# Performance work log

Hardware: AMD Instinct MI355X
Metric: run time of the kernel (lower is better)

## Reference

```python
import jax, jax.numpy as jnp
import numpy as np

B = 256          # batch_size (number of graphs)
N = 512          # padded nodes per graph
IN_FEATS = 74
DIM = 128
E = 1_048_576    # total edges in batched graph
N_NODES = B * N


def setup_inputs() -> dict:
    key = jax.random.key(0)
    ks = jax.random.split(key, 10)
    x = jax.random.normal(ks[0], (N_NODES, IN_FEATS), dtype=jnp.float32)
    src = jax.random.randint(ks[1], (E,), 0, N_NODES, dtype=jnp.int32)
    dst = jax.random.randint(ks[2], (E,), 0, N_NODES, dtype=jnp.int32)
    # init_transform: Linear(in_feats, dim_embedding, bias=False); padding=True
    # zeroes weight[-1] (last OUTPUT row) -> last column in [in, out] layout.
    W_init = jax.random.normal(ks[3], (IN_FEATS, DIM), dtype=jnp.float32) * 0.1
    W_init = W_init.at[:, -1].set(0.0)
    W1 = jax.random.normal(ks[4], (DIM, DIM), dtype=jnp.float32) * 0.1
    W2 = jax.random.normal(ks[5], (DIM, DIM), dtype=jnp.float32) * 0.1
    W3 = jax.random.normal(ks[6], (DIM, DIM), dtype=jnp.float32) * 0.1
    b1 = jnp.zeros((DIM,), dtype=jnp.float32)
    b2 = jnp.zeros((DIM,), dtype=jnp.float32)
    b3 = jnp.zeros((DIM,), dtype=jnp.float32)
    return {"x": x, "src": src, "dst": dst, "W_init": W_init,
            "W1": W1, "b1": b1, "W2": W2, "b2": b2, "W3": W3, "b3": b3}


def _gcn_forward(x, src, dst, W_init, Ws, bs):
    n = x.shape[0]
    h = x @ W_init                                    # [n, DIM] initial embedding
    ones = jnp.ones(src.shape[0], dtype=x.dtype)
    deg_out = jax.ops.segment_sum(ones, src, num_segments=n)
    deg_in = jax.ops.segment_sum(ones, dst, num_segments=n)
    nrm_src = jax.lax.rsqrt(jnp.clip(deg_out, 1.0))   # D_out^{-1/2}
    nrm_dst = jax.lax.rsqrt(jnp.clip(deg_in, 1.0))    # D_in^{-1/2}
    for W, b in zip(Ws, bs):
        m = (h * nrm_src[:, None])[src]               # gather normalized messages [E, DIM]
        agg = jax.ops.segment_sum(m, dst, num_segments=n)  # scatter-add to dst nodes
        h = jax.nn.relu((agg * nrm_dst[:, None]) @ W + b)
    return h.reshape(B, N, -1)                        # [B, N, output_feats]


def reference(x, src, dst, W_init, W1, b1, W2, b2, W3, b3):
    return _gcn_forward(x, src, dst, W_init, (W1, W2, W3), (b1, b2, b3))
```

## Files before the change

### kernel.cpp

```cpp
#include <hip/hip_runtime.h>

#define NN 131072
#define NE 1048576
#define OFF_DEG_OUT 0x000000
#define OFF_CURSOR  0x080000
#define OFF_WT      0x100000
#define OFF_WTI     0x118000
#define OFF_BUCKET  0x200000
#define OFF_HN      0x2200000

typedef __attribute__((ext_vector_type(8))) short bf16x8;
typedef __attribute__((ext_vector_type(4))) float f32x4;

static __device__ __forceinline__ float blo(unsigned u){ return __uint_as_float(u << 16); }
static __device__ __forceinline__ float bhi(unsigned u){ return __uint_as_float(u & 0xffff0000u); }
static __device__ __forceinline__ unsigned f2b(float f){
    unsigned u = __float_as_uint(f);
    return (u + 0x7fffu + ((u >> 16) & 1u)) >> 16;
}
static __device__ __forceinline__ unsigned pack2(float a, float b){
    return f2b(a) | (f2b(b) << 16);
}

__global__ __launch_bounds__(256) void k_fill(const int* __restrict__ src,
                                              const int* __restrict__ dst,
                                              int* __restrict__ deg_out,
                                              int* __restrict__ cursor,
                                              int* __restrict__ bucket) {
    int base = (blockIdx.x * 256 + threadIdx.x) * 2;
    int2 s2 = *(const int2*)&src[base];
    int2 d2 = *(const int2*)&dst[base];
    int p0 = atomicAdd(&cursor[d2.x], 1);
    int p1 = atomicAdd(&cursor[d2.y], 1);
    atomicAdd(&deg_out[s2.x], 1);
    atomicAdd(&deg_out[s2.y], 1);
    if (p0 < 64) bucket[(size_t)d2.x * 64 + p0] = s2.x;
    if (p1 < 64) bucket[(size_t)d2.y * 64 + p1] = s2.y;
}

__global__ __launch_bounds__(256) void k_wprep(const float* __restrict__ W1,
                                               const float* __restrict__ W2,
                                               const float* __restrict__ W3,
                                               const float* __restrict__ Wi,
                                               unsigned short* __restrict__ Wt,
                                               unsigned short* __restrict__ Wti) {
    int idx = blockIdx.x * 256 + threadIdx.x;
    if (idx < 49152) {
        int L = idx >> 14, rem = idx & 16383;
        int k = rem >> 7, n = rem & 127;
        const float* W = L == 0 ? W1 : (L == 1 ? W2 : W3);
        Wt[L * 16384 + n * 128 + k] = (unsigned short)f2b(W[k * 128 + n]);
    } else if (idx < 61440) {
        int rem = idx - 49152;
        int n = rem / 96, k = rem - n * 96;
        float v = (k < 74) ? Wi[k * 128 + n] : 0.f;
        Wti[n * 96 + k] = (unsigned short)f2b(v);
    }
}

__global__ __launch_bounds__(256) void k_init(const float* __restrict__ X,
                                              const unsigned short* __restrict__ Wti,
                                              const int* __restrict__ deg_out,
                                              unsigned short* __restrict__ hn) {
    __shared__ unsigned int xs[64 * 68];
    int tid = threadIdx.x;
    int m0 = blockIdx.x * 64;

    for (int idx = tid; idx < 2368; idx += 256) {
        int m = idx / 37, t = idx - m * 37;
        float2 v = *(const float2*)&X[(size_t)(m0 + m) * 74 + t * 2];
        xs[m * 68 + t] = pack2(v.x, v.y);
    }
    for (int idx = tid; idx < 64 * 11; idx += 256) {
        int m = idx / 11, c = 37 + idx % 11;
        xs[m * 68 + c] = 0u;
    }
    __syncthreads();

    int wave = tid >> 6, lane = tid & 63, quad = lane >> 4, l16 = lane & 15;
    f32x4 acc[8];
    #pragma unroll
    for (int t = 0; t < 8; ++t) acc[t] = (f32x4){0.f, 0.f, 0.f, 0.f};
    int arow = (wave * 16 + l16) * 68 + quad * 4;
    #pragma unroll
    for (int ks = 0; ks < 3; ++ks) {
        bf16x8 af = *(const bf16x8*)&xs[arow + ks * 16];
        #pragma unroll
        for (int t = 0; t < 8; ++t) {
            bf16x8 bf = *(const bf16x8*)(Wti + (t * 16 + l16) * 96 + ks * 32 + quad * 8);
            acc[t] = __builtin_amdgcn_mfma_f32_16x16x32_bf16(af, bf, acc[t], 0, 0, 0);
        }
    }
    __syncthreads();
    unsigned short* atb = (unsigned short*)xs;
    int mb = wave * 16 + quad * 4;
    float nsr[4];
    #pragma unroll
    for (int r = 0; r < 4; ++r) {
        int dq = deg_out[m0 + mb + r];
        nsr[r] = rsqrtf((float)(dq > 1 ? dq : 1));
    }
    #pragma unroll
    for (int t = 0; t < 8; ++t)
        #pragma unroll
        for (int r = 0; r < 4; ++r)
            atb[(mb + r) * 136 + t * 16 + l16] = (unsigned short)f2b(acc[t][r] * nsr[r]);
    __syncthreads();
    {
        int r = tid >> 2, c0 = (tid & 3) * 32;
        unsigned int* sp = &xs[r * 68 + (tid & 3) * 16];
        #pragma unroll
        for (int j = 0; j < 4; ++j)
            *(uint4*)(hn + (size_t)(m0 + r) * 128 + c0 + j * 8) = *(const uint4*)(sp + j * 4);
    }
}

__global__ __launch_bounds__(256) void k_layer(const uint4* __restrict__ hn4,
                                               const int* __restrict__ bucket,
                                               const int* __restrict__ deg_in,
                                               const int* __restrict__ deg_out,
                                               const unsigned short* __restrict__ Wt,
                                               const float* __restrict__ bias,
                                               void* __restrict__ OutP, int last) {
    __shared__ unsigned int at[64 * 68];
    int tid = threadIdx.x;
    int m0 = blockIdx.x * 64;

    int g = tid >> 4, l16p = tid & 15;
    #pragma unroll
    for (int pass = 0; pass < 4; ++pass) {
        int nl = pass * 16 + g;
        int n = m0 + nl;
        int cnt = deg_in[n];
        cnt = cnt < 64 ? cnt : 64;
        const int* brow = bucket + (size_t)n * 64;
        float a0 = 0, a1 = 0, a2 = 0, a3 = 0, a4 = 0, a5 = 0, a6 = 0, a7 = 0;
        for (int c = 0; c < cnt; c += 8) {
            int4 sA = *(const int4*)&brow[c];
            int4 sB = *(const int4*)&brow[c + 4];
            int lim = cnt - c;
            int i1 = lim > 1 ? sA.y : 0;
            int i2 = lim > 2 ? sA.z : 0;
            int i3 = lim > 3 ? sA.w : 0;
            int i4 = lim > 4 ? sB.x : 0;
            int i5 = lim > 5 ? sB.y : 0;
            int i6 = lim > 6 ? sB.z : 0;
            int i7 = lim > 7 ? sB.w : 0;
            uint4 v0 = hn4[(size_t)sA.x * 16 + l16p];
            uint4 v1 = hn4[(size_t)i1 * 16 + l16p];
            uint4 v2 = hn4[(size_t)i2 * 16 + l16p];
            uint4 v3 = hn4[(size_t)i3 * 16 + l16p];
            uint4 v4 = hn4[(size_t)i4 * 16 + l16p];
            uint4 v5 = hn4[(size_t)i5 * 16 + l16p];
            uint4 v6 = hn4[(size_t)i6 * 16 + l16p];
            uint4 v7 = hn4[(size_t)i7 * 16 + l16p];
            float w1 = lim > 1 ? 1.f : 0.f;
            float w2 = lim > 2 ? 1.f : 0.f;
            float w3 = lim > 3 ? 1.f : 0.f;
            float w4 = lim > 4 ? 1.f : 0.f;
            float w5 = lim > 5 ? 1.f : 0.f;
            float w6 = lim > 6 ? 1.f : 0.f;
            float w7 = lim > 7 ? 1.f : 0.f;
            a0 += blo(v0.x); a1 += bhi(v0.x); a2 += blo(v0.y); a3 += bhi(v0.y);
            a4 += blo(v0.z); a5 += bhi(v0.z); a6 += blo(v0.w); a7 += bhi(v0.w);
            a0 = fmaf(w1, blo(v1.x), a0); a1 = fmaf(w1, bhi(v1.x), a1);
            a2 = fmaf(w1, blo(v1.y), a2); a3 = fmaf(w1, bhi(v1.y), a3);
            a4 = fmaf(w1, blo(v1.z), a4); a5 = fmaf(w1, bhi(v1.z), a5);
            a6 = fmaf(w1, blo(v1.w), a6); a7 = fmaf(w1, bhi(v1.w), a7);
            a0 = fmaf(w2, blo(v2.x), a0); a1 = fmaf(w2, bhi(v2.x), a1);
            a2 = fmaf(w2, blo(v2.y), a2); a3 = fmaf(w2, bhi(v2.y), a3);
            a4 = fmaf(w2, blo(v2.z), a4); a5 = fmaf(w2, bhi(v2.z), a5);
            a6 = fmaf(w2, blo(v2.w), a6); a7 = fmaf(w2, bhi(v2.w), a7);
            a0 = fmaf(w3, blo(v3.x), a0); a1 = fmaf(w3, bhi(v3.x), a1);
            a2 = fmaf(w3, blo(v3.y), a2); a3 = fmaf(w3, bhi(v3.y), a3);
            a4 = fmaf(w3, blo(v3.z), a4); a5 = fmaf(w3, bhi(v3.z), a5);
            a6 = fmaf(w3, blo(v3.w), a6); a7 = fmaf(w3, bhi(v3.w), a7);
            a0 = fmaf(w4, blo(v4.x), a0); a1 = fmaf(w4, bhi(v4.x), a1);
            a2 = fmaf(w4, blo(v4.y), a2); a3 = fmaf(w4, bhi(v4.y), a3);
            a4 = fmaf(w4, blo(v4.z), a4); a5 = fmaf(w4, bhi(v4.z), a5);
            a6 = fmaf(w4, blo(v4.w), a6); a7 = fmaf(w4, bhi(v4.w), a7);
            a0 = fmaf(w5, blo(v5.x), a0); a1 = fmaf(w5, bhi(v5.x), a1);
            a2 = fmaf(w5, blo(v5.y), a2); a3 = fmaf(w5, bhi(v5.y), a3);
            a4 = fmaf(w5, blo(v5.z), a4); a5 = fmaf(w5, bhi(v5.z), a5);
            a6 = fmaf(w5, blo(v5.w), a6); a7 = fmaf(w5, bhi(v5.w), a7);
            a0 = fmaf(w6, blo(v6.x), a0); a1 = fmaf(w6, bhi(v6.x), a1);
            a2 = fmaf(w6, blo(v6.y), a2); a3 = fmaf(w6, bhi(v6.y), a3);
            a4 = fmaf(w6, blo(v6.z), a4); a5 = fmaf(w6, bhi(v6.z), a5);
            a6 = fmaf(w6, blo(v6.w), a6); a7 = fmaf(w6, bhi(v6.w), a7);
            a0 = fmaf(w7, blo(v7.x), a0); a1 = fmaf(w7, bhi(v7.x), a1);
            a2 = fmaf(w7, blo(v7.y), a2); a3 = fmaf(w7, bhi(v7.y), a3);
            a4 = fmaf(w7, blo(v7.z), a4); a5 = fmaf(w7, bhi(v7.z), a5);
            a6 = fmaf(w7, blo(v7.w), a6); a7 = fmaf(w7, bhi(v7.w), a7);
        }
        float nd = rsqrtf((float)(cnt > 1 ? cnt : 1));
        uint4 o;
        o.x = pack2(a0 * nd, a1 * nd); o.y = pack2(a2 * nd, a3 * nd);
        o.z = pack2(a4 * nd, a5 * nd); o.w = pack2(a6 * nd, a7 * nd);
        *(uint4*)&at[nl * 68 + l16p * 4] = o;
    }
    __syncthreads();

    f32x4 acc[8];
    #pragma unroll
    for (int t = 0; t < 8; ++t) acc[t] = (f32x4){0.f, 0.f, 0.f, 0.f};
    int wave = tid >> 6, lane = tid & 63, quad = lane >> 4, l16 = lane & 15;
    int arow = (wave * 16 + l16) * 68 + quad * 4;
    #pragma unroll
    for (int ks = 0; ks < 4; ++ks) {
        bf16x8 af = *(const bf16x8*)&at[arow + ks * 16];
        #pragma unroll
        for (int t = 0; t < 8; ++t) {
            bf16x8 bf = *(const bf16x8*)(Wt + (t * 16 + l16) * 128 + ks * 32 + quad * 8);
            acc[t] = __builtin_amdgcn_mfma_f32_16x16x32_bf16(af, bf, acc[t], 0, 0, 0);
        }
    }

    int mb = wave * 16 + quad * 4;
    if (!last) {
        float nsr[4];
        #pragma unroll
        for (int r = 0; r < 4; ++r) {
            int dq = deg_out[m0 + mb + r];
            nsr[r] = rsqrtf((float)(dq > 1 ? dq : 1));
        }
        __syncthreads();
        unsigned short* atb = (unsigned short*)at;
        #pragma unroll
        for (int t = 0; t < 8; ++t) {
            float bv = bias[t * 16 + l16];
            #pragma unroll
            for (int r = 0; r < 4; ++r) {
                float v = acc[t][r] + bv;
                v = (v > 0.f ? v : 0.f) * nsr[r];
                atb[(mb + r) * 136 + t * 16 + l16] = (unsigned short)f2b(v);
            }
        }
        __syncthreads();
        int r = tid >> 2, c0 = (tid & 3) * 32;
        unsigned short* Out = (unsigned short*)OutP;
        unsigned int* sp = &at[r * 68 + (tid & 3) * 16];
        #pragma unroll
        for (int j = 0; j < 4; ++j)
            *(uint4*)(Out + (size_t)(m0 + r) * 128 + c0 + j * 8) = *(const uint4*)(sp + j * 4);
    } else {
        float* Out = (float*)OutP;
        #pragma unroll
        for (int t = 0; t < 8; ++t) {
            float bv = bias[t * 16 + l16];
            #pragma unroll
            for (int r = 0; r < 4; ++r) {
                float v = acc[t][r] + bv;
                v = v > 0.f ? v : 0.f;
                Out[(size_t)(m0 + mb + r) * 128 + t * 16 + l16] = v;
            }
        }
    }
}

extern "C" void kernel_launch(void* const* d_in, const int* in_sizes, int n_in,
                              void* d_out, int out_size, void* d_ws, size_t ws_size,
                              hipStream_t stream) {
    const float* x  = (const float*)d_in[0];
    const int* src  = (const int*)d_in[1];
    const int* dst  = (const int*)d_in[2];
    const float* Wi = (const float*)d_in[3];
    const float* W1 = (const float*)d_in[4];
    const float* b1 = (const float*)d_in[5];
    const float* W2 = (const float*)d_in[6];
    const float* b2 = (const float*)d_in[7];
    const float* W3 = (const float*)d_in[8];
    const float* b3 = (const float*)d_in[9];

    char* ws = (char*)d_ws;
    int* deg_out   = (int*)(ws + OFF_DEG_OUT);
    int* cursor    = (int*)(ws + OFF_CURSOR);
    unsigned short* Wt  = (unsigned short*)(ws + OFF_WT);
    unsigned short* Wti = (unsigned short*)(ws + OFF_WTI);
    int* bucket    = (int*)(ws + OFF_BUCKET);
    unsigned short* hnA = (unsigned short*)(ws + OFF_HN);
    unsigned short* hnB = (unsigned short*)d_out;

    hipMemsetAsync(ws, 0, 0x100000, stream);
    k_fill<<<NE / 512, 256, 0, stream>>>(src, dst, deg_out, cursor, bucket);
    k_wprep<<<240, 256, 0, stream>>>(W1, W2, W3, Wi, Wt, Wti);
    k_init<<<NN / 64, 256, 0, stream>>>(x, Wti, deg_out, hnA);

    const float* bl[3] = {b1, b2, b3};
    k_layer<<<NN / 64, 256, 0, stream>>>((const uint4*)hnA, bucket, cursor, deg_out,
                                         Wt,         bl[0], (void*)hnB, 0);
    k_layer<<<NN / 64, 256, 0, stream>>>((const uint4*)hnB, bucket, cursor, deg_out,
                                         Wt + 16384, bl[1], (void*)hnA, 0);
    k_layer<<<NN / 64, 256, 0, stream>>>((const uint4*)hnA, bucket, cursor, deg_out,
                                         Wt + 32768, bl[2], d_out, 1);
}
```

Baseline: 446.0 us.

## Quantize node features to int8 with per-row scales for gathers

Node embeddings between layers are now stored as 8-bit values with a per-row float scale. The first layer uses signed int8 and the post-ReLU layers use unsigned uint8. This halves the bytes moved by the random neighbour gathers, which dominate the aggregation, at the cost of an extra scale load per edge and lower numerical precision that may exceed tolerance. The workspace memset is also folded into the weight-prep kernel to remove one launch.

Measured after the change: 406.0 us. 9.0% less time.

```diff
diff --git a/kernel.cpp b/kernel.cpp
--- a/kernel.cpp
+++ b/kernel.cpp
@@ -8,6 +8,8 @@
 #define OFF_WTI     0x118000
 #define OFF_BUCKET  0x200000
 #define OFF_HN      0x2200000
+#define OFF_SCA     0x3200000
+#define OFF_SCB     0x3280000
 
 typedef __attribute__((ext_vector_type(8))) short bf16x8;
 typedef __attribute__((ext_vector_type(4))) float f32x4;
@@ -20,6 +22,9 @@
 }
 static __device__ __forceinline__ unsigned pack2(float a, float b){
     return f2b(a) | (f2b(b) << 16);
+}
+static __device__ __forceinline__ unsigned packq(int q0, int q1, int q2, int q3){
+    return (q0 & 255) | ((q1 & 255) << 8) | ((q2 & 255) << 16) | ((q3 & 255) << 24);
 }
 
 __global__ __launch_bounds__(256) void k_fill(const int* __restrict__ src,
@@ -43,8 +48,10 @@
                                                const float* __restrict__ W3,
                                                const float* __restrict__ Wi,
                                                unsigned short* __restrict__ Wt,
-                                               unsigned short* __restrict__ Wti) {
+                                               unsigned short* __restrict__ Wti,
+                                               uint4* __restrict__ zdst) {
     int idx = blockIdx.x * 256 + threadIdx.x;
+    zdst[idx] = (uint4){0u, 0u, 0u, 0u};
     if (idx < 49152) {
         int L = idx >> 14, rem = idx & 16383;
         int k = rem >> 7, n = rem & 127;
@@ -61,7 +68,8 @@
 __global__ __launch_bounds__(256) void k_init(const float* __restrict__ X,
                                               const unsigned short* __restrict__ Wti,
                                               const int* __restrict__ deg_out,
-                                              unsigned short* __restrict__ hn) {
+                                              unsigned char* __restrict__ hn,
+                                              float* __restrict__ scInv) {
     __shared__ unsigned int xs[64 * 68];
     int tid = threadIdx.x;
     int m0 = blockIdx.x * 64;
@@ -107,21 +115,65 @@
             atb[(mb + r) * 136 + t * 16 + l16] = (unsigned short)f2b(acc[t][r] * nsr[r]);
     __syncthreads();
     {
-        int r = tid >> 2, c0 = (tid & 3) * 32;
-        unsigned int* sp = &xs[r * 68 + (tid & 3) * 16];
-        #pragma unroll
-        for (int j = 0; j < 4; ++j)
-            *(uint4*)(hn + (size_t)(m0 + r) * 128 + c0 + j * 8) = *(const uint4*)(sp + j * 4);
-    }
-}
-
-__global__ __launch_bounds__(256) void k_layer(const uint4* __restrict__ hn4,
+        int r = tid >> 2, cg = tid & 3;
+        const unsigned int* sp = &xs[r * 68 + cg * 16];
+        float v[32]; float am = 0.f;
+        #pragma unroll
+        for (int j = 0; j < 16; ++j) {
+            unsigned u = sp[j];
+            float e = blo(u), o = bhi(u);
+            v[2 * j] = e; v[2 * j + 1] = o;
+            am = fmaxf(am, fmaxf(fabsf(e), fabsf(o)));
+        }
+        am = fmaxf(am, __shfl_xor(am, 1));
+        am = fmaxf(am, __shfl_xor(am, 2));
+        float scl = am > 1e-30f ? 127.f / am : 0.f;
+        if (cg == 0) scInv[m0 + r] = am * (1.f / 127.f);
+        unsigned w[8];
+        #pragma unroll
+        for (int j = 0; j < 8; ++j)
+            w[j] = packq((int)rintf(v[4 * j] * scl),     (int)rintf(v[4 * j + 1] * scl),
+                         (int)rintf(v[4 * j + 2] * scl), (int)rintf(v[4 * j + 3] * scl));
+        uint4* op = (uint4*)(hn + (size_t)(m0 + r) * 128 + cg * 32);
+        op[0] = (uint4){w[0], w[1], w[2], w[3]};
+        op[1] = (uint4){w[4], w[5], w[6], w[7]};
+    }
+}
+
+#define DEQS8(vv, ss) do {                                                     \
+    unsigned ux = (vv).x, uy = (vv).y;                                         \
+    a0 = fmaf((ss), (float)(int)(signed char)(ux),       a0);                  \
+    a1 = fmaf((ss), (float)(int)(signed char)(ux >> 8),  a1);                  \
+    a2 = fmaf((ss), (float)(int)(signed char)(ux >> 16), a2);                  \
+    a3 = fmaf((ss), (float)(int)(signed char)(ux >> 24), a3);                  \
+    a4 = fmaf((ss), (float)(int)(signed char)(uy),       a4);                  \
+    a5 = fmaf((ss), (float)(int)(signed char)(uy >> 8),  a5);                  \
+    a6 = fmaf((ss), (float)(int)(signed char)(uy >> 16), a6);                  \
+    a7 = fmaf((ss), (float)(int)(signed char)(uy >> 24), a7);                  \
+} while (0)
+
+#define DEQU8(vv, ss) do {                                                     \
+    unsigned ux = (vv).x, uy = (vv).y;                                         \
+    a0 = fmaf((ss), (float)(ux & 255),         a0);                            \
+    a1 = fmaf((ss), (float)((ux >> 8) & 255),  a1);                            \
+    a2 = fmaf((ss), (float)((ux >> 16) & 255), a2);                            \
+    a3 = fmaf((ss), (float)(ux >> 24),         a3);                            \
+    a4 = fmaf((ss), (float)(uy & 255),         a4);                            \
+    a5 = fmaf((ss), (float)((uy >> 8) & 255),  a5);                            \
+    a6 = fmaf((ss), (float)((uy >> 16) & 255), a6);                            \
+    a7 = fmaf((ss), (float)(uy >> 24),         a7);                            \
+} while (0)
+
+template<int USRC>
+__global__ __launch_bounds__(256) void k_layer(const uint2* __restrict__ hn2,
+                                               const float* __restrict__ sc,
                                                const int* __restrict__ bucket,
                                                const int* __restrict__ deg_in,
                                                const int* __restrict__ deg_out,
                                                const unsigned short* __restrict__ Wt,
                                                const float* __restrict__ bias,
-                                               void* __restrict__ OutP, int last) {
+                                               void* __restrict__ OutP,
+                                               float* __restrict__ scOut, int last) {
     __shared__ unsigned int at[64 * 68];
     int tid = threadIdx.x;
     int m0 = blockIdx.x * 64;
@@ -146,51 +198,29 @@
             int i5 = lim > 5 ? sB.y : 0;
             int i6 = lim > 6 ? sB.z : 0;
             int i7 = lim > 7 ? sB.w : 0;
-            uint4 v0 = hn4[(size_t)sA.x * 16 + l16p];
-            uint4 v1 = hn4[(size_t)i1 * 16 + l16p];
-            uint4 v2 = hn4[(size_t)i2 * 16 + l16p];
-            uint4 v3 = hn4[(size_t)i3 * 16 + l16p];
-            uint4 v4 = hn4[(size_t)i4 * 16 + l16p];
-            uint4 v5 = hn4[(size_t)i5 * 16 + l16p];
-            uint4 v6 = hn4[(size_t)i6 * 16 + l16p];
-            uint4 v7 = hn4[(size_t)i7 * 16 + l16p];
-            float w1 = lim > 1 ? 1.f : 0.f;
-            float w2 = lim > 2 ? 1.f : 0.f;
-            float w3 = lim > 3 ? 1.f : 0.f;
-            float w4 = lim > 4 ? 1.f : 0.f;
-            float w5 = lim > 5 ? 1.f : 0.f;
-            float w6 = lim > 6 ? 1.f : 0.f;
-            float w7 = lim > 7 ? 1.f : 0.f;
-            a0 += blo(v0.x); a1 += bhi(v0.x); a2 += blo(v0.y); a3 += bhi(v0.y);
-            a4 += blo(v0.z); a5 += bhi(v0.z); a6 += blo(v0.w); a7 += bhi(v0.w);
-            a0 = fmaf(w1, blo(v1.x), a0); a1 = fmaf(w1, bhi(v1.x), a1);
-            a2 = fmaf(w1, blo(v1.y), a2); a3 = fmaf(w1, bhi(v1.y), a3);
-            a4 = fmaf(w1, blo(v1.z), a4); a5 = fmaf(w1, bhi(v1.z), a5);
-            a6 = fmaf(w1, blo(v1.w), a6); a7 = fmaf(w1, bhi(v1.w), a7);
-            a0 = fmaf(w2, blo(v2.x), a0); a1 = fmaf(w2, bhi(v2.x), a1);
-            a2 = fmaf(w2, blo(v2.y), a2); a3 = fmaf(w2, bhi(v2.y), a3);
-            a4 = fmaf(w2, blo(v2.z), a4); a5 = fmaf(w2, bhi(v2.z), a5);
-            a6 = fmaf(w2, blo(v2.w), a6); a7 = fmaf(w2, bhi(v2.w), a7);
-            a0 = fmaf(w3, blo(v3.x), a0); a1 = fmaf(w3, bhi(v3.x), a1);
-            a2 = fmaf(w3, blo(v3.y), a2); a3 = fmaf(w3, bhi(v3.y), a3);
-            a4 = fmaf(w3, blo(v3.z), a4); a5 = fmaf(w3, bhi(v3.z), a5);
-            a6 = fmaf(w3, blo(v3.w), a6); a7 = fmaf(w3, bhi(v3.w), a7);
-            a0 = fmaf(w4, blo(v4.x), a0); a1 = fmaf(w4, bhi(v4.x), a1);
-            a2 = fmaf(w4, blo(v4.y), a2); a3 = fmaf(w4, bhi(v4.y), a3);
-            a4 = fmaf(w4, blo(v4.z), a4); a5 = fmaf(w4, bhi(v4.z), a5);
-            a6 = fmaf(w4, blo(v4.w), a6); a7 = fmaf(w4, bhi(v4.w), a7);
-            a0 = fmaf(w5, blo(v5.x), a0); a1 = fmaf(w5, bhi(v5.x), a1);
-            a2 = fmaf(w5, blo(v5.y), a2); a3 = fmaf(w5, bhi(v5.y), a3);
-            a4 = fmaf(w5, blo(v5.z), a4); a5 = fmaf(w5, bhi(v5.z), a5);
-            a6 = fmaf(w5, blo(v5.w), a6); a7 = fmaf(w5, bhi(v5.w), a7);
-            a0 = fmaf(w6, blo(v6.x), a0); a1 = fmaf(w6, bhi(v6.x), a1);
-            a2 = fmaf(w6, blo(v6.y), a2); a3 = fmaf(w6, bhi(v6.y), a3);
-            a4 = fmaf(w6, blo(v6.z), a4); a5 = fmaf(w6, bhi(v6.z), a5);
-            a6 = fmaf(w6, blo(v6.w), a6); a7 = fmaf(w6, bhi(v6.w), a7);
-            a0 = fmaf(w7, blo(v7.x), a0); a1 = fmaf(w7, bhi(v7.x), a1);
-            a2 = fmaf(w7, blo(v7.y), a2); a3 = fmaf(w7, bhi(v7.y), a3);
-            a4 = fmaf(w7, blo(v7.z), a4); a5 = fmaf(w7, bhi(v7.z), a5);
-            a6 = fmaf(w7, blo(v7.w), a6); a7 = fmaf(w7, bhi(v7.w), a7);
+            uint2 v0 = hn2[(size_t)sA.x * 16 + l16p];
+            uint2 v1 = hn2[(size_t)i1 * 16 + l16p];
+            uint2 v2 = hn2[(size_t)i2 * 16 + l16p];
+            uint2 v3 = hn2[(size_t)i3 * 16 + l16p];
+            uint2 v4 = hn2[(size_t)i4 * 16 + l16p];
+            uint2 v5 = hn2[(size_t)i5 * 16 + l16p];
+            uint2 v6 = hn2[(size_t)i6 * 16 + l16p];
+            uint2 v7 = hn2[(size_t)i7 * 16 + l16p];
+            float s0 = sc[sA.x];
+            float s1 = sc[i1]; s1 = lim > 1 ? s1 : 0.f;
+            float s2 = sc[i2]; s2 = lim > 2 ? s2 : 0.f;
+            float s3 = sc[i3]; s3 = lim > 3 ? s3 : 0.f;
+            float s4 = sc[i4]; s4 = lim > 4 ? s4 : 0.f;
+            float s5 = sc[i5]; s5 = lim > 5 ? s5 : 0.f;
+            float s6 = sc[i6]; s6 = lim > 6 ? s6 : 0.f;
+            float s7 = sc[i7]; s7 = lim > 7 ? s7 : 0.f;
+            if (USRC) {
+                DEQU8(v0, s0); DEQU8(v1, s1); DEQU8(v2, s2); DEQU8(v3, s3);
+                DEQU8(v4, s4); DEQU8(v5, s5); DEQU8(v6, s6); DEQU8(v7, s7);
+            } else {
+                DEQS8(v0, s0); DEQS8(v1, s1); DEQS8(v2, s2); DEQS8(v3, s3);
+                DEQS8(v4, s4); DEQS8(v5, s5); DEQS8(v6, s6); DEQS8(v7, s7);
+            }
         }
         float nd = rsqrtf((float)(cnt > 1 ? cnt : 1));
         uint4 o;
@@ -236,12 +266,29 @@
             }
         }
         __syncthreads();
-        int r = tid >> 2, c0 = (tid & 3) * 32;
-        unsigned short* Out = (unsigned short*)OutP;
-        unsigned int* sp = &at[r * 68 + (tid & 3) * 16];
-        #pragma unroll
-        for (int j = 0; j < 4; ++j)
-            *(uint4*)(Out + (size_t)(m0 + r) * 128 + c0 + j * 8) = *(const uint4*)(sp + j * 4);
+        int r = tid >> 2, cg = tid & 3;
+        const unsigned int* sp = &at[r * 68 + cg * 16];
+        float v[32]; float am = 0.f;
+        #pragma unroll
+        for (int j = 0; j < 16; ++j) {
+            unsigned u = sp[j];
+            float e = blo(u), o = bhi(u);
+            v[2 * j] = e; v[2 * j + 1] = o;
+            am = fmaxf(am, fmaxf(e, o));
+        }
+        am = fmaxf(am, __shfl_xor(am, 1));
+        am = fmaxf(am, __shfl_xor(am, 2));
+        float scl = am > 1e-30f ? 254.f / am : 0.f;
+        if (cg == 0) scOut[m0 + r] = am * (1.f / 254.f);
+        unsigned w[8];
+        #pragma unroll
+        for (int j = 0; j < 8; ++j)
+            w[j] = packq((int)rintf(v[4 * j] * scl),     (int)rintf(v[4 * j + 1] * scl),
+                         (int)rintf(v[4 * j + 2] * scl), (int)rintf(v[4 * j + 3] * scl));
+        unsigned char* Out = (unsigned char*)OutP;
+        uint4* op = (uint4*)(Out + (size_t)(m0 + r) * 128 + cg * 32);
+        op[0] = (uint4){w[0], w[1], w[2], w[3]};
+        op[1] = (uint4){w[4], w[5], w[6], w[7]};
     } else {
         float* Out = (float*)OutP;
         #pragma unroll
@@ -277,19 +324,19 @@
     unsigned short* Wt  = (unsigned short*)(ws + OFF_WT);
     unsigned short* Wti = (unsigned short*)(ws + OFF_WTI);
     int* bucket    = (int*)(ws + OFF_BUCKET);
-    unsigned short* hnA = (unsigned short*)(ws + OFF_HN);
-    unsigned short* hnB = (unsigned short*)d_out;
-
-    hipMemsetAsync(ws, 0, 0x100000, stream);
+    unsigned char* hnA = (unsigned char*)(ws + OFF_HN);
+    float* scA     = (float*)(ws + OFF_SCA);
+    float* scB     = (float*)(ws + OFF_SCB);
+    unsigned char* hnB = (unsigned char*)d_out;
+
+    k_wprep<<<256, 256, 0, stream>>>(W1, W2, W3, Wi, Wt, Wti, (uint4*)ws);
     k_fill<<<NE / 512, 256, 0, stream>>>(src, dst, deg_out, cursor, bucket);
-    k_wprep<<<240, 256, 0, stream>>>(W1, W2, W3, Wi, Wt, Wti);
-    k_init<<<NN / 64, 256, 0, stream>>>(x, Wti, deg_out, hnA);
-
-    const float* bl[3] = {b1, b2, b3};
-    k_layer<<<NN / 64, 256, 0, stream>>>((const uint4*)hnA, bucket, cursor, deg_out,
-                                         Wt,         bl[0], (void*)hnB, 0);
-    k_layer<<<NN / 64, 256, 0, stream>>>((const uint4*)hnB, bucket, cursor, deg_out,
-                                         Wt + 16384, bl[1], (void*)hnA, 0);
-    k_layer<<<NN / 64, 256, 0, stream>>>((const uint4*)hnA, bucket, cursor, deg_out,
-                                         Wt + 32768, bl[2], d_out, 1);
-}
+    k_init<<<NN / 64, 256, 0, stream>>>(x, Wti, deg_out, hnA, scA);
+
+    k_layer<0><<<NN / 64, 256, 0, stream>>>((const uint2*)hnA, scA, bucket, cursor, deg_out,
+                                            Wt,         b1, (void*)hnB, scB, 0);
+    k_layer<1><<<NN / 64, 256, 0, stream>>>((const uint2*)hnB, scB, bucket, cursor, deg_out,
+                                            Wt + 16384, b2, (void*)hnA, scA, 0);
+    k_layer<1><<<NN / 64, 256, 0, stream>>>((const uint2*)hnA, scA, bucket, cursor, deg_out,
+                                            Wt + 32768, b3, d_out, nullptr, 1);
+}
```
